# Optimization experiments

Measured on AMD Instinct MI355X. Metric: run time of the kernel, lower is better.

The kernel has to match this reference:

```python
import jax, jax.numpy as jnp
import numpy as np

C = 16      # internal_channel
DG = 8      # deform groups
KK = 9      # 3x3 kernel


def conv2d(x, w, b, pad):
    out = jax.lax.conv_general_dilated(
        x, w, (1, 1), [(pad, pad), (pad, pad)],
        dimension_numbers=('NCHW', 'OIHW', 'NCHW'))
    return out + b[None, :, None, None]


def feature_extraction(img, w1, b1, w2, b2, w3, b3):
    f1 = jax.nn.relu(conv2d(img, w1, b1, 1))   # [B,C,H,W]
    f2 = jax.nn.relu(conv2d(f1, w2, b2, 0))    # [B,C,H-2,W-2]
    f3 = jax.nn.relu(conv2d(f2, w3, b3, 0))    # [B,C,H-4,W-4]
    return [f1, f2, f3]


def deform_conv(x, offset, w, b):
    # x: [B,C,H,W]; offset: [B, DG*KK*2, H, W] (y,x pairs); w: [Cout,C,3,3]
    B, Cin, H, W = x.shape
    Cg = Cin // DG
    off = offset.reshape(B, DG, KK, 2, H, W)
    ky = jnp.repeat(jnp.arange(3) - 1, 3)  # kernel y offsets (pad=1)
    kx = jnp.tile(jnp.arange(3) - 1, 3)
    base_y = jnp.arange(H).reshape(1, 1, 1, H, 1)
    base_x = jnp.arange(W).reshape(1, 1, 1, 1, W)
    sy = base_y + ky.reshape(1, 1, KK, 1, 1) + off[:, :, :, 0]  # [B,DG,KK,H,W]
    sx = base_x + kx.reshape(1, 1, KK, 1, 1) + off[:, :, :, 1]
    y0 = jnp.floor(sy)
    x0 = jnp.floor(sx)
    wy = (sy - y0)[:, :, None]  # [B,DG,1,KK,H,W]
    wx = (sx - x0)[:, :, None]
    y0i = y0.astype(jnp.int32)
    x0i = x0.astype(jnp.int32)
    xg = x.reshape(B, DG, Cg, H * W)

    def gather(yy, xx):
        valid = (yy >= 0) & (yy < H) & (xx >= 0) & (xx < W)  # zero pad outside
        idx = (jnp.clip(yy, 0, H - 1) * W + jnp.clip(xx, 0, W - 1))
        idx_b = jnp.broadcast_to(idx.reshape(B, DG, 1, KK, H * W), (B, DG, Cg, KK, H * W))
        src = jnp.broadcast_to(xg[:, :, :, None, :], (B, DG, Cg, KK, H * W))
        g = jnp.take_along_axis(src, idx_b, axis=-1).reshape(B, DG, Cg, KK, H, W)
        return g * valid[:, :, None].astype(x.dtype)

    v00 = gather(y0i, x0i)
    v01 = gather(y0i, x0i + 1)
    v10 = gather(y0i + 1, x0i)
    v11 = gather(y0i + 1, x0i + 1)
    s = (v00 * (1 - wy) * (1 - wx) + v01 * (1 - wy) * wx
         + v10 * wy * (1 - wx) + v11 * wy * wx)
    s = s.reshape(B, Cin, KK, H, W)
    out = jnp.einsum('bckhw,ock->bohw', s, w.reshape(w.shape[0], Cin, KK))
    return out + b[None, :, None, None]


def setup_inputs() -> dict:
    key = jax.random.key(0)
    ks = jax.random.split(key, 24)
    B, H, W = 4, 192, 192
    sc = 0.05
    d = {
        'ref_image': jax.random.normal(ks[0], (B, C, H, W), jnp.float32),
        'unreg_image': jax.random.normal(ks[1], (B, C, H, W), jnp.float32),
        'fe_w1': jax.random.normal(ks[2], (C, C, 3, 3), jnp.float32) * sc,
        'fe_b1': jnp.zeros((C,), jnp.float32),
        'fe_w2': jax.random.normal(ks[3], (C, C, 3, 3), jnp.float32) * sc,
        'fe_b2': jnp.zeros((C,), jnp.float32),
        'fe_w3': jax.random.normal(ks[4], (C, C, 3, 3), jnp.float32) * sc,
        'fe_b3': jnp.zeros((C,), jnp.float32),
        'off_w0': jax.random.normal(ks[5], (C, 2 * C, 3, 3), jnp.float32) * sc,
        'off_b0': jnp.zeros((C,), jnp.float32),
        'off_w1': jax.random.normal(ks[6], (C, 2 * C, 3, 3), jnp.float32) * sc,
        'off_b1': jnp.zeros((C,), jnp.float32),
        'off_w2': jax.random.normal(ks[7], (C, 2 * C, 3, 3), jnp.float32) * sc,
        'off_b2': jnp.zeros((C,), jnp.float32),
        'dcn_off_w': jax.random.normal(ks[8], (2 * DG * KK, C, 3, 3), jnp.float32) * sc,
        'dcn_off_b': jnp.zeros((2 * DG * KK,), jnp.float32),
        'dcn_w': jax.random.normal(ks[9], (C, C, 3, 3), jnp.float32) * sc,
        'dcn_b': jnp.zeros((C,), jnp.float32),
    }
    return d


def reference(ref_image, unreg_image, fe_w1, fe_b1, fe_w2, fe_b2, fe_w3, fe_b3,
              off_w0, off_b0, off_w1, off_b1, off_w2, off_b2,
              dcn_off_w, dcn_off_b, dcn_w, dcn_b):
    ref_f = feature_extraction(ref_image, fe_w1, fe_b1, fe_w2, fe_b2, fe_w3, fe_b3)
    unr_f = feature_extraction(unreg_image, fe_w1, fe_b1, fe_w2, fe_b2, fe_w3, fe_b3)
    off_ws = [(off_w0, off_b0), (off_w1, off_b1), (off_w2, off_b2)]
    aligned = [None, None, None]
    for i in range(2, -1, -1):  # coarse-to-fine as in the source loop
        cat = jnp.concatenate([ref_f[i], unr_f[i]], axis=1)        # [B,2C,h,w]
        off_feat = jax.nn.relu(conv2d(cat, off_ws[i][0], off_ws[i][1], 1))
        offsets = conv2d(off_feat, dcn_off_w, dcn_off_b, 1)        # [B,2*DG*KK,h,w]
        aligned[i] = deform_conv(unr_f[i], offsets, dcn_w, dcn_b)
    return tuple(aligned)
```

## Files before the change

### kernel.cpp

```cpp
#include <hip/hip_runtime.h>

typedef unsigned int uint;
typedef unsigned short ushort;
typedef __attribute__((ext_vector_type(8))) short bf16x8;
typedef __attribute__((ext_vector_type(4))) float f32x4;

__device__ inline ushort f2bf(float f) {
    uint u = __float_as_uint(f);
    u += 0x7fff + ((u >> 16) & 1);
    return (ushort)(u >> 16);
}
__device__ inline float bflo(uint w) { return __uint_as_float(w << 16); }
__device__ inline float bfhi(uint w) { return __uint_as_float(w & 0xffff0000u); }

__global__ void packall_k(
    const float* __restrict__ fe_w1, const float* __restrict__ fe_w2,
    const float* __restrict__ fe_w3, const float* __restrict__ off_w0,
    const float* __restrict__ off_w1, const float* __restrict__ off_w2,
    const float* __restrict__ dcn_off_w, const float* __restrict__ dcn_w,
    ushort* __restrict__ pf1, ushort* __restrict__ pf2, ushort* __restrict__ pf3,
    ushort* __restrict__ po0, ushort* __restrict__ po1, ushort* __restrict__ po2,
    ushort* __restrict__ pow_, ushort* __restrict__ pd) {
    const int y = blockIdx.y;
    int i = blockIdx.x * 256 + threadIdx.x;
    const float* w; ushort* pk; int CIN, NT, KS;
    switch (y) {
        case 0: w = fe_w1;  pk = pf1;  CIN = 16; NT = 1; KS = 5; break;
        case 1: w = fe_w2;  pk = pf2;  CIN = 16; NT = 1; KS = 5; break;
        case 2: w = fe_w3;  pk = pf3;  CIN = 16; NT = 1; KS = 5; break;
        case 3: w = off_w0; pk = po0;  CIN = 32; NT = 1; KS = 9; break;
        case 4: w = off_w1; pk = po1;  CIN = 32; NT = 1; KS = 9; break;
        case 5: w = off_w2; pk = po2;  CIN = 32; NT = 1; KS = 9; break;
        case 6: w = dcn_off_w; pk = pow_; CIN = 16; NT = 9; KS = 5; break;
        default: w = dcn_w; pk = pd;   CIN = 16; NT = 1; KS = 5; break;
    }
    if (i >= KS * NT * 512) return;
    int e = i & 7, lane = (i >> 3) & 63, rest = i >> 9;
    int nt = rest % NT, ks = rest / NT;
    int k = ks * 32 + (lane >> 4) * 8 + e;
    int n = nt * 16 + (lane & 15);
    int t, ci;
    if (CIN == 16) { t = k >> 4; ci = k & 15; } else { t = k >> 5; ci = k & 31; }
    float v = (t < 9) ? w[(n * CIN + ci) * 9 + t] : 0.f;
    pk[i] = f2bf(v);
}

template <bool PLANAR>
__launch_bounds__(256)
__global__ void fe_mfma_k(const float* __restrict__ pA, const float* __restrict__ pB,
                          const ushort* __restrict__ catin,
                          const ushort* __restrict__ pack, const float* __restrict__ bias,
                          ushort* __restrict__ catout,
                          int H, int W, int OH, int OW, int pad) {
    __shared__ ushort patch[324 * 16];
    const int tid = threadIdx.x;
    const int tx0 = blockIdx.x * 16, ty0 = blockIdx.y * 16;
    const int b = blockIdx.z & 3, img = blockIdx.z >> 2;
    const int bx = tx0 - pad, by = ty0 - pad;
    const int HW = H * W;

    if (PLANAR) {
        const float* inb = (img ? pB : pA) + (size_t)(b * 16) * HW;
        for (int pos = tid; pos < 324; pos += 256) {
            int r = pos / 18, c = pos - r * 18;
            int gy = by + r, gx = bx + c;
            bool ok = (unsigned)gy < (unsigned)H && (unsigned)gx < (unsigned)W;
            int base = gy * W + gx;
            uint o16[8];
#pragma unroll
            for (int ii = 0; ii < 8; ++ii) {
                float lo = ok ? inb[(2 * ii) * HW + base] : 0.f;
                float hi = ok ? inb[(2 * ii + 1) * HW + base] : 0.f;
                o16[ii] = (uint)f2bf(lo) | ((uint)f2bf(hi) << 16);
            }
            *(uint4*)(patch + pos * 16) = *(uint4*)&o16[0];
            *(uint4*)(patch + pos * 16 + 8) = *(uint4*)&o16[4];
        }
    } else {
        for (int c = tid; c < 648; c += 256) {
            int pos = c >> 1, h = c & 1;
            int r = pos / 18, col = pos - r * 18;
            int gy = by + r, gx = bx + col;
            uint4 v = make_uint4(0, 0, 0, 0);
            if ((unsigned)gy < (unsigned)H && (unsigned)gx < (unsigned)W)
                v = *(const uint4*)(catin + ((size_t)(b * H + gy) * W + gx) * 32 + img * 16 + h * 8);
            *(uint4*)(patch + pos * 16 + h * 8) = v;
        }
    }
    __syncthreads();

    const int lane = tid & 63, wv = tid >> 6;
    const int g = lane >> 4, ci0 = (g & 1) * 8, rowx = lane & 15;
    f32x4 acc[4];
    float bv = bias[rowx];
#pragma unroll
    for (int m = 0; m < 4; ++m) acc[m] = f32x4{bv, bv, bv, bv};

#pragma unroll
    for (int ks = 0; ks < 5; ++ks) {
        int t = 2 * ks + (g >> 1);
        int dy = t < 9 ? t / 3 : 0;
        int dx = t < 9 ? t - (t / 3) * 3 : 0;
        bf16x8 a[4];
#pragma unroll
        for (int m = 0; m < 4; ++m) {
            int r = wv * 4 + m + dy, cc = rowx + dx;
            a[m] = *(const bf16x8*)(patch + (r * 18 + cc) * 16 + ci0);
        }
        bf16x8 bfrag = *(const bf16x8*)((const uint4*)pack + ks * 64 + lane);
#pragma unroll
        for (int m = 0; m < 4; ++m)
            acc[m] = __builtin_amdgcn_mfma_f32_16x16x32_bf16(a[m], bfrag, acc[m], 0, 0, 0);
    }

    const int oxb = g * 4;
#pragma unroll
    for (int m = 0; m < 4; ++m) {
        int gy = ty0 + wv * 4 + m;
        if (gy >= OH) continue;
#pragma unroll
        for (int j = 0; j < 4; ++j) {
            int gx = tx0 + oxb + j;
            if (gx < OW)
                catout[((size_t)(b * OH + gy) * OW + gx) * 32 + img * 16 + rowx] =
                    f2bf(fmaxf(acc[m][j], 0.f));
        }
    }
}

__launch_bounds__(256)
__global__ void off_mfma_k(const ushort* __restrict__ c0, const ushort* __restrict__ c1,
                           const ushort* __restrict__ c2,
                           const ushort* __restrict__ pk0, const ushort* __restrict__ pk1,
                           const ushort* __restrict__ pk2,
                           const float* __restrict__ b0, const float* __restrict__ b1,
                           const float* __restrict__ b2,
                           ushort* __restrict__ f0, ushort* __restrict__ f1,
                           ushort* __restrict__ f2) {
    const int z = blockIdx.z, s = z >> 2, b = z & 3;
    const int H = 192 - 2 * s, W = H;
    const ushort* cat  = s == 0 ? c0 : (s == 1 ? c1 : c2);
    const ushort* pack = s == 0 ? pk0 : (s == 1 ? pk1 : pk2);
    const float* bias  = s == 0 ? b0 : (s == 1 ? b1 : b2);
    ushort* out        = s == 0 ? f0 : (s == 1 ? f1 : f2);

    __shared__ ushort patch[324 * 32];
    const int tid = threadIdx.x;
    const int tx0 = blockIdx.x * 16, ty0 = blockIdx.y * 16;
    const int bx = tx0 - 1, by = ty0 - 1;

    for (int c = tid; c < 1296; c += 256) {
        int pos = c >> 2, h = c & 3;
        int r = pos / 18, col = pos - r * 18;
        int gy = by + r, gx = bx + col;
        uint4 v = make_uint4(0, 0, 0, 0);
        if ((unsigned)gy < (unsigned)H && (unsigned)gx < (unsigned)W)
            v = *(const uint4*)(cat + ((size_t)(b * H + gy) * W + gx) * 32 + h * 8);
        *(uint4*)(patch + pos * 32 + h * 8) = v;
    }
    __syncthreads();

    const int lane = tid & 63, wv = tid >> 6;
    const int g = lane >> 4, ci0 = g * 8, rowx = lane & 15;
    f32x4 acc[4];
    float bv = bias[rowx];
#pragma unroll
    for (int m = 0; m < 4; ++m) acc[m] = f32x4{bv, bv, bv, bv};

#pragma unroll
    for (int ks = 0; ks < 9; ++ks) {
        int dy = ks / 3, dx = ks - (ks / 3) * 3;
        bf16x8 a[4];
#pragma unroll
        for (int m = 0; m < 4; ++m) {
            int r = wv * 4 + m + dy, cc = rowx + dx;
            a[m] = *(const bf16x8*)(patch + (r * 18 + cc) * 32 + ci0);
        }
        bf16x8 bfrag = *(const bf16x8*)((const uint4*)pack + ks * 64 + lane);
#pragma unroll
        for (int m = 0; m < 4; ++m)
            acc[m] = __builtin_amdgcn_mfma_f32_16x16x32_bf16(a[m], bfrag, acc[m], 0, 0, 0);
    }

    const int oxb = g * 4;
#pragma unroll
    for (int m = 0; m < 4; ++m) {
        int gy = ty0 + wv * 4 + m;
        if (gy >= H) continue;
#pragma unroll
        for (int j = 0; j < 4; ++j) {
            int gx = tx0 + oxb + j;
            if (gx < W)
                out[((size_t)(b * H + gy) * W + gx) * 16 + rowx] = f2bf(fmaxf(acc[m][j], 0.f));
        }
    }
}

__launch_bounds__(256)
__global__ void dcn_fused_k(const ushort* __restrict__ c0, const ushort* __restrict__ c1,
                            const ushort* __restrict__ c2,
                            const ushort* __restrict__ fb0, const ushort* __restrict__ fb1,
                            const ushort* __restrict__ fb2,
                            const ushort* __restrict__ owPack, const float* __restrict__ ob,
                            const ushort* __restrict__ pd, const float* __restrict__ db,
                            float* __restrict__ o0, float* __restrict__ o1,
                            float* __restrict__ o2) {
    const int z = blockIdx.z;
    const int s = z >> 2, b = z & 3;
    const int H = 192 - 2 * s, W = H;
    const ushort* cat = s == 0 ? c0 : (s == 1 ? c1 : c2);
    const ushort* fb  = s == 0 ? fb0 : (s == 1 ? fb1 : fb2);
    float* out        = s == 0 ? o0 : (s == 1 ? o1 : o2);
    const int HW = H * W;
    const size_t pixb = (size_t)b * HW;

    __shared__ ushort smem[26240];
    ushort* patch = smem;
    float2* xt = (float2*)(smem + 10752);

    const int tid = threadIdx.x;
    const int tx0 = blockIdx.x * 16, ty0 = blockIdx.y * 16;

    for (int c = tid; c < 648; c += 256) {
        int pos = c >> 1, h = c & 1;
        int r = pos / 18, col = pos - r * 18;
        int gy = ty0 - 1 + r, gx = tx0 - 1 + col;
        uint4 v = make_uint4(0, 0, 0, 0);
        if ((unsigned)gy < (unsigned)H && (unsigned)gx < (unsigned)W)
            v = *(const uint4*)(fb + ((size_t)(b * H + gy) * W + gx) * 16 + h * 8);
        *(uint4*)(patch + pos * 16 + h * 8) = v;
    }
    {
        const int bx3 = tx0 - 3, by3 = ty0 - 3;
        for (int pos = tid; pos < 484; pos += 256) {
            int r = pos / 22, c = pos - r * 22;
            int gy2 = by3 + r, gx2 = bx3 + c;
            uint4 va = make_uint4(0, 0, 0, 0), vb = va;
            if ((unsigned)gy2 < (unsigned)H && (unsigned)gx2 < (unsigned)W) {
                const ushort* src = cat + (pixb + gy2 * W + gx2) * 32 + 16;
                va = *(const uint4*)src;
                vb = *(const uint4*)(src + 8);
            }
            uint u[8] = {va.x, va.y, va.z, va.w, vb.x, vb.y, vb.z, vb.w};
#pragma unroll
            for (int cp = 0; cp < 8; ++cp)
                xt[cp * 484 + pos] = make_float2(bflo(u[cp]), bfhi(u[cp]));
        }
    }
    __syncthreads();

    const int lane = tid & 63, wv = tid >> 6;
    const int g = lane >> 4, rowx = lane & 15, half = g & 1;
    const int ci0 = half * 8;

    f32x4 acc[4][9];
#pragma unroll
    for (int n = 0; n < 9; ++n) {
        float bv = ob[n * 16 + rowx];
#pragma unroll
        for (int m = 0; m < 4; ++m) acc[m][n] = f32x4{bv, bv, bv, bv};
    }

#pragma unroll
    for (int ks = 0; ks < 5; ++ks) {
        int t = 2 * ks + (g >> 1);
        int dy = t < 9 ? t / 3 : 0;
        int dx = t < 9 ? t - (t / 3) * 3 : 0;
        bf16x8 a[4];
#pragma unroll
        for (int m = 0; m < 4; ++m) {
            int r = wv * 4 + m + dy, cc = rowx + dx;
            a[m] = *(const bf16x8*)(patch + (r * 18 + cc) * 16 + ci0);
        }
        const uint4* bp = (const uint4*)owPack + (size_t)(ks * 9) * 64 + lane;
#pragma unroll
        for (int n = 0; n < 9; ++n) {
            bf16x8 bfrag = *(const bf16x8*)(bp + (size_t)n * 64);
#pragma unroll
            for (int m = 0; m < 4; ++m)
                acc[m][n] = __builtin_amdgcn_mfma_f32_16x16x32_bf16(a[m], bfrag, acc[m][n], 0, 0, 0);
        }
    }
    __syncthreads();

    ushort* ot = smem + wv * 2688;
    const int px = tx0 + rowx;
    const float bv2 = db[rowx];

#pragma unroll
    for (int m = 0; m < 4; ++m) {
#pragma unroll
        for (int n = 0; n < 9; ++n) {
            int ch = n * 16 + rowx;
            int dg = ch / 18;
            int rem = ch - dg * 18;
            int col = (rem >> 1) * 16 + dg * 2 + (rem & 1);
#pragma unroll
            for (int j = 0; j < 4; ++j)
                ot[(g * 4 + j) * 168 + col] = f2bf(acc[m][n][j]);
        }

        const int py = ty0 + wv * 4 + m;
        f32x4 acc2 = f32x4{bv2, bv2, bv2, bv2};

#pragma unroll 1
        for (int ks = 0; ks < 5; ++ks) {
            const int t = 2 * ks + (g >> 1);
            const bool tv = (t < 9);
            const int t3 = t / 3;
            const int ky = (tv ? t3 : 0) - 1, kx = (tv ? t - t3 * 3 : 0) - 1;

            uint a2[4];
            if (tv) {
                uint4 ov = *(const uint4*)(ot + rowx * 168 + t * 16 + half * 8);
                uint ovv[4] = {ov.x, ov.y, ov.z, ov.w};
#pragma unroll
                for (int d = 0; d < 4; ++d) {
                    const int dgA = half * 4 + d;
                    uint u = ovv[d];
                    float sy = (float)(py + ky) + bflo(u);
                    float sx = (float)(px + kx) + bfhi(u);
                    float fy = floorf(sy), fx = floorf(sx);
                    int y0 = (int)fy, x0 = (int)fx;
                    float wy = sy - fy, wx = sx - fx;
                    float wy1 = 1.f - wy, wx1 = 1.f - wx;
                    float w00 = wy1 * wx1, w01 = wy1 * wx, w10 = wy * wx1, w11 = wy * wx;
                    int ly = y0 - (ty0 - 3), lx = x0 - (tx0 - 3);
                    float2 v00, v01, v10, v11;
                    if ((unsigned)ly <= 20u && (unsigned)lx <= 20u) {
                        const float2* tt = &xt[dgA * 484 + ly * 22 + lx];
                        v00 = tt[0]; v01 = tt[1]; v10 = tt[22]; v11 = tt[23];
                    } else {
                        v00 = v01 = v10 = v11 = make_float2(0.f, 0.f);
                        bool y0v = (unsigned)y0 < (unsigned)H;
                        bool y1v = (unsigned)(y0 + 1) < (unsigned)H;
                        bool x0v = (unsigned)x0 < (unsigned)W;
                        bool x1v = (unsigned)(x0 + 1) < (unsigned)W;
                        const ushort* cg = cat + ((size_t)pixb + (size_t)y0 * W + x0) * 32 + 16 + 2 * dgA;
                        if (y0v && x0v) { uint uu = *(const uint*)cg;                 v00 = make_float2(bflo(uu), bfhi(uu)); }
                        if (y0v && x1v) { uint uu = *(const uint*)(cg + 32);          v01 = make_float2(bflo(uu), bfhi(uu)); }
                        if (y1v && x0v) { uint uu = *(const uint*)(cg + 32 * W);      v10 = make_float2(bflo(uu), bfhi(uu)); }
                        if (y1v && x1v) { uint uu = *(const uint*)(cg + 32 * W + 32); v11 = make_float2(bflo(uu), bfhi(uu)); }
                    }
                    float s0 = w00 * v00.x + w01 * v01.x + w10 * v10.x + w11 * v11.x;
                    float s1 = w00 * v00.y + w01 * v01.y + w10 * v10.y + w11 * v11.y;
                    a2[d] = (uint)f2bf(s0) | ((uint)f2bf(s1) << 16);
                }
            } else {
                a2[0] = a2[1] = a2[2] = a2[3] = 0u;
            }
            uint4 av = make_uint4(a2[0], a2[1], a2[2], a2[3]);
            bf16x8 af = *(bf16x8*)&av;
            bf16x8 dfrag = *(const bf16x8*)((const uint4*)pd + ks * 64 + lane);
            acc2 = __builtin_amdgcn_mfma_f32_16x16x32_bf16(af, dfrag, acc2, 0, 0, 0);
        }

        if (py < H) {
            float* op = out + (size_t)(b * 16 + rowx) * HW + (size_t)py * W;
#pragma unroll
            for (int j = 0; j < 4; ++j) {
                int gx2 = tx0 + g * 4 + j;
                if (gx2 < W) op[gx2] = acc2[j];
            }
        }
    }
}

extern "C" void kernel_launch(void* const* d_in, const int* in_sizes, int n_in,
                              void* d_out, int out_size, void* d_ws, size_t ws_size,
                              hipStream_t stream) {
    const float* ref_image = (const float*)d_in[0];
    const float* unreg_image = (const float*)d_in[1];
    const float* fe_w1 = (const float*)d_in[2];
    const float* fe_b1 = (const float*)d_in[3];
    const float* fe_w2 = (const float*)d_in[4];
    const float* fe_b2 = (const float*)d_in[5];
    const float* fe_w3 = (const float*)d_in[6];
    const float* fe_b3 = (const float*)d_in[7];
    const float* off_w0 = (const float*)d_in[8];
    const float* off_b0 = (const float*)d_in[9];
    const float* off_w1 = (const float*)d_in[10];
    const float* off_b1 = (const float*)d_in[11];
    const float* off_w2 = (const float*)d_in[12];
    const float* off_b2 = (const float*)d_in[13];
    const float* dcn_off_w = (const float*)d_in[14];
    const float* dcn_off_b = (const float*)d_in[15];
    const float* dcn_w = (const float*)d_in[16];
    const float* dcn_b = (const float*)d_in[17];

    const size_t pix[3] = {4ul * 192 * 192, 4ul * 190 * 190, 4ul * 188 * 188};
    const size_t szf[3] = {pix[0] * 16, pix[1] * 16, pix[2] * 16};

    size_t o = 0;
    auto take = [&](size_t bytes) {
        void* r = (char*)d_ws + o;
        o += (bytes + 255) & ~(size_t)255;
        return r;
    };
    ushort* cat[3]; ushort* fb[3];
    ushort* pf[3]; ushort* po[3]; ushort* owPack; ushort* pd;
    for (int s = 0; s < 3; ++s) cat[s] = (ushort*)take(pix[s] * 32 * 2);
    for (int s = 0; s < 3; ++s) fb[s] = (ushort*)take(pix[s] * 16 * 2);
    for (int s = 0; s < 3; ++s) pf[s] = (ushort*)take(2560 * 2);
    for (int s = 0; s < 3; ++s) po[s] = (ushort*)take(4608 * 2);
    owPack = (ushort*)take(23040 * 2);
    pd = (ushort*)take(2560 * 2);

    float* out0 = (float*)d_out;
    float* out1 = out0 + szf[0];
    float* out2 = out1 + szf[1];

    dim3 blk(256);

    packall_k<<<dim3(90, 8), blk, 0, stream>>>(
        fe_w1, fe_w2, fe_w3, off_w0, off_w1, off_w2, dcn_off_w, dcn_w,
        pf[0], pf[1], pf[2], po[0], po[1], po[2], owPack, pd);

    fe_mfma_k<true><<<dim3(12, 12, 8), blk, 0, stream>>>(
        ref_image, unreg_image, nullptr, pf[0], fe_b1, cat[0], 192, 192, 192, 192, 1);
    fe_mfma_k<false><<<dim3(12, 12, 8), blk, 0, stream>>>(
        nullptr, nullptr, cat[0], pf[1], fe_b2, cat[1], 192, 192, 190, 190, 0);
    fe_mfma_k<false><<<dim3(12, 12, 8), blk, 0, stream>>>(
        nullptr, nullptr, cat[1], pf[2], fe_b3, cat[2], 190, 190, 188, 188, 0);

    off_mfma_k<<<dim3(12, 12, 12), blk, 0, stream>>>(
        cat[0], cat[1], cat[2], po[0], po[1], po[2],
        off_b0, off_b1, off_b2, fb[0], fb[1], fb[2]);

    dcn_fused_k<<<dim3(12, 12, 12), blk, 0, stream>>>(
        cat[0], cat[1], cat[2], fb[0], fb[1], fb[2],
        owPack, dcn_off_b, pd, dcn_b, out0, out1, out2);
}
```

Measured before the change: 196.8 us.

## Interleave offset conv per row to cut registers and shared memory for occupancy

The fused DCN kernel now computes the offset-conv accumulators one output row at a time inside the row loop, instead of holding all 36 f32x4 accumulators live. It stores the input sampling tile as packed bf16 pairs rather than expanded float2 and gives the offset tile its own smaller buffer, which shrinks LDS. It also sets launch bounds to 3 blocks per CU and preloads the dcn weight fragments into registers. The intent is to raise occupancy and overlap the MFMA and gather phases, at the cost of extra bf16 unpacking in the inner gather loop and less MFMA batching per A fragment.

Result: slower. 359.2 us (+82.6%).

```diff
diff --git a/kernel.cpp b/kernel.cpp
--- a/kernel.cpp
+++ b/kernel.cpp
@@ -196,7 +196,7 @@
     }
 }
 
-__launch_bounds__(256)
+__launch_bounds__(256, 3)
 __global__ void dcn_fused_k(const ushort* __restrict__ c0, const ushort* __restrict__ c1,
                             const ushort* __restrict__ c2,
                             const ushort* __restrict__ fb0, const ushort* __restrict__ fb1,
@@ -214,9 +214,9 @@
     const int HW = H * W;
     const size_t pixb = (size_t)b * HW;
 
-    __shared__ ushort smem[26240];
-    ushort* patch = smem;
-    float2* xt = (float2*)(smem + 10752);
+    __shared__ ushort patch[324 * 16];
+    __shared__ uint   xtu[8 * 484];
+    __shared__ ushort ot[4 * 16 * 152];
 
     const int tid = threadIdx.x;
     const int tx0 = blockIdx.x * 16, ty0 = blockIdx.y * 16;
@@ -241,10 +241,10 @@
                 va = *(const uint4*)src;
                 vb = *(const uint4*)(src + 8);
             }
-            uint u[8] = {va.x, va.y, va.z, va.w, vb.x, vb.y, vb.z, vb.w};
-#pragma unroll
-            for (int cp = 0; cp < 8; ++cp)
-                xt[cp * 484 + pos] = make_float2(bflo(u[cp]), bfhi(u[cp]));
+            xtu[0 * 484 + pos] = va.x; xtu[1 * 484 + pos] = va.y;
+            xtu[2 * 484 + pos] = va.z; xtu[3 * 484 + pos] = va.w;
+            xtu[4 * 484 + pos] = vb.x; xtu[5 * 484 + pos] = vb.y;
+            xtu[6 * 484 + pos] = vb.z; xtu[7 * 484 + pos] = vb.w;
         }
     }
     __syncthreads();
@@ -252,43 +252,41 @@
     const int lane = tid & 63, wv = tid >> 6;
     const int g = lane >> 4, rowx = lane & 15, half = g & 1;
     const int ci0 = half * 8;
-
-    f32x4 acc[4][9];
-#pragma unroll
-    for (int n = 0; n < 9; ++n) {
-        float bv = ob[n * 16 + rowx];
-#pragma unroll
-        for (int m = 0; m < 4; ++m) acc[m][n] = f32x4{bv, bv, bv, bv};
-    }
-
-#pragma unroll
-    for (int ks = 0; ks < 5; ++ks) {
-        int t = 2 * ks + (g >> 1);
-        int dy = t < 9 ? t / 3 : 0;
-        int dx = t < 9 ? t - (t / 3) * 3 : 0;
-        bf16x8 a[4];
-#pragma unroll
-        for (int m = 0; m < 4; ++m) {
-            int r = wv * 4 + m + dy, cc = rowx + dx;
-            a[m] = *(const bf16x8*)(patch + (r * 18 + cc) * 16 + ci0);
-        }
-        const uint4* bp = (const uint4*)owPack + (size_t)(ks * 9) * 64 + lane;
-#pragma unroll
-        for (int n = 0; n < 9; ++n) {
-            bf16x8 bfrag = *(const bf16x8*)(bp + (size_t)n * 64);
-#pragma unroll
-            for (int m = 0; m < 4; ++m)
-                acc[m][n] = __builtin_amdgcn_mfma_f32_16x16x32_bf16(a[m], bfrag, acc[m][n], 0, 0, 0);
-        }
-    }
-    __syncthreads();
-
-    ushort* ot = smem + wv * 2688;
     const int px = tx0 + rowx;
     const float bv2 = db[rowx];
-
-#pragma unroll
+    ushort* otw = ot + wv * (16 * 152);
+
+    bf16x8 pdv0 = *(const bf16x8*)((const uint4*)pd + 0 * 64 + lane);
+    bf16x8 pdv1 = *(const bf16x8*)((const uint4*)pd + 1 * 64 + lane);
+    bf16x8 pdv2 = *(const bf16x8*)((const uint4*)pd + 2 * 64 + lane);
+    bf16x8 pdv3 = *(const bf16x8*)((const uint4*)pd + 3 * 64 + lane);
+    bf16x8 pdv4 = *(const bf16x8*)((const uint4*)pd + 4 * 64 + lane);
+
+#pragma unroll 1
     for (int m = 0; m < 4; ++m) {
+        const int py = ty0 + wv * 4 + m;
+
+        f32x4 acc[9];
+#pragma unroll
+        for (int n = 0; n < 9; ++n) {
+            float bv = ob[n * 16 + rowx];
+            acc[n] = f32x4{bv, bv, bv, bv};
+        }
+#pragma unroll
+        for (int ks = 0; ks < 5; ++ks) {
+            int t = 2 * ks + (g >> 1);
+            int dy = t < 9 ? t / 3 : 0;
+            int dx = t < 9 ? t - (t / 3) * 3 : 0;
+            int r = wv * 4 + m + dy, cc = rowx + dx;
+            bf16x8 a = *(const bf16x8*)(patch + (r * 18 + cc) * 16 + ci0);
+            const uint4* bp = (const uint4*)owPack + (size_t)(ks * 9) * 64 + lane;
+#pragma unroll
+            for (int n = 0; n < 9; ++n) {
+                bf16x8 bfrag = *(const bf16x8*)(bp + (size_t)n * 64);
+                acc[n] = __builtin_amdgcn_mfma_f32_16x16x32_bf16(a, bfrag, acc[n], 0, 0, 0);
+            }
+        }
+
 #pragma unroll
         for (int n = 0; n < 9; ++n) {
             int ch = n * 16 + rowx;
@@ -297,13 +295,11 @@
             int col = (rem >> 1) * 16 + dg * 2 + (rem & 1);
 #pragma unroll
             for (int j = 0; j < 4; ++j)
-                ot[(g * 4 + j) * 168 + col] = f2bf(acc[m][n][j]);
-        }
-
-        const int py = ty0 + wv * 4 + m;
+                otw[(g * 4 + j) * 152 + col] = f2bf(acc[n][j]);
+        }
+
         f32x4 acc2 = f32x4{bv2, bv2, bv2, bv2};
-
-#pragma unroll 1
+#pragma unroll
         for (int ks = 0; ks < 5; ++ks) {
             const int t = 2 * ks + (g >> 1);
             const bool tv = (t < 9);
@@ -312,7 +308,7 @@
 
             uint a2[4];
             if (tv) {
-                uint4 ov = *(const uint4*)(ot + rowx * 168 + t * 16 + half * 8);
+                uint4 ov = *(const uint4*)(otw + rowx * 152 + t * 16 + half * 8);
                 uint ovv[4] = {ov.x, ov.y, ov.z, ov.w};
 #pragma unroll
                 for (int d = 0; d < 4; ++d) {
@@ -328,8 +324,12 @@
                     int ly = y0 - (ty0 - 3), lx = x0 - (tx0 - 3);
                     float2 v00, v01, v10, v11;
                     if ((unsigned)ly <= 20u && (unsigned)lx <= 20u) {
-                        const float2* tt = &xt[dgA * 484 + ly * 22 + lx];
-                        v00 = tt[0]; v01 = tt[1]; v10 = tt[22]; v11 = tt[23];
+                        const uint* tt = &xtu[dgA * 484 + ly * 22 + lx];
+                        uint u00 = tt[0], u01 = tt[1], u10 = tt[22], u11 = tt[23];
+                        v00 = make_float2(bflo(u00), bfhi(u00));
+                        v01 = make_float2(bflo(u01), bfhi(u01));
+                        v10 = make_float2(bflo(u10), bfhi(u10));
+                        v11 = make_float2(bflo(u11), bfhi(u11));
                     } else {
                         v00 = v01 = v10 = v11 = make_float2(0.f, 0.f);
                         bool y0v = (unsigned)y0 < (unsigned)H;
@@ -351,7 +351,8 @@
             }
             uint4 av = make_uint4(a2[0], a2[1], a2[2], a2[3]);
             bf16x8 af = *(bf16x8*)&av;
-            bf16x8 dfrag = *(const bf16x8*)((const uint4*)pd + ks * 64 + lane);
+            bf16x8 dfrag = ks == 0 ? pdv0 : ks == 1 ? pdv1 : ks == 2 ? pdv2
+                         : ks == 3 ? pdv3 : pdv4;
             acc2 = __builtin_amdgcn_mfma_f32_16x16x32_bf16(af, dfrag, acc2, 0, 0, 0);
         }
 
```
